# Optimization experiments

Measured on AMD Instinct MI355X. Metric: run time of the kernel, lower is better.

The kernel has to match this reference:

```python
import jax, jax.numpy as jnp
import numpy as np

D_MODEL = 2048
NUM_HEADS = 16
HEAD_DIM = D_MODEL // NUM_HEADS
BATCH = 2
SEQ = 2048


def setup_inputs() -> dict:
    key = jax.random.key(0)
    ks = jax.random.split(key, 5)
    s = 1.0 / np.sqrt(D_MODEL)
    return {
        "x": jax.random.normal(ks[0], (BATCH, SEQ, D_MODEL), dtype=jnp.float32),
        "Wq": jax.random.normal(ks[1], (D_MODEL, D_MODEL), dtype=jnp.float32) * s,
        "Wk": jax.random.normal(ks[2], (D_MODEL, D_MODEL), dtype=jnp.float32) * s,
        "Wv": jax.random.normal(ks[3], (D_MODEL, D_MODEL), dtype=jnp.float32) * s,
        "Wo": jax.random.normal(ks[4], (D_MODEL, D_MODEL), dtype=jnp.float32) * s,
    }


def reference(x, Wq, Wk, Wv, Wo):
    B, S, D = x.shape
    H, Dh = NUM_HEADS, HEAD_DIM
    # nn.Linear(bias=False): y = x @ W.T ; split_heads is a plain view (no transpose!)
    Q = (x @ Wq.T).reshape(B, H, S, Dh)
    K = (x @ Wk.T).reshape(B, H, S, Dh)
    V = (x @ Wv.T).reshape(B, H, S, Dh)
    # scores scaled by head_dim (NOT sqrt) — faithful to source
    scores = jnp.einsum("bhqd,bhkd->bhqk", Q, K) / jnp.float32(Dh)
    causal_mask = jnp.triu(jnp.ones((S, S), dtype=bool), k=1)  # True above diagonal
    scores = jnp.where(causal_mask, -jnp.inf, scores)
    attn = jax.nn.softmax(scores, axis=-1)
    out = jnp.einsum("bhqk,bhkd->bhqd", attn, V)  # [B,H,S,Dh]
    out = out.transpose(0, 2, 1, 3).reshape(B, S, D)  # merge DOES transpose
    return out @ Wo.T
```

## Files before the change

### kernel.cpp

```cpp
#include <hip/hip_runtime.h>
#include <hip/hip_bf16.h>

using bf16 = __hip_bfloat16;
typedef __attribute__((ext_vector_type(8))) short bf16x8;
typedef __attribute__((ext_vector_type(4))) float f32x4;

#define DEVI __device__ __forceinline__

constexpr int Bn = 2, Sn = 2048, Dn = 2048, Hn = 16, DHn = 128;
constexpr int Mn = Bn * Sn;

DEVI void gload_lds16(const bf16* g, bf16* l) {
  __builtin_amdgcn_global_load_lds(
      (__attribute__((address_space(1))) void*)g,
      (__attribute__((address_space(3))) void*)l,
      16, 0, 0);
}

__global__ __launch_bounds__(256) void cvt_bf16_k(const float* __restrict__ in,
                                                  bf16* __restrict__ out, int n8) {
  int i = blockIdx.x * 256 + threadIdx.x;
  if (i >= n8) return;
  const float4* p = (const float4*)in + (size_t)i * 2;
  float4 a = p[0], b = p[1];
  union { bf16 h[8]; bf16x8 v; } u;
  u.h[0] = __float2bfloat16(a.x); u.h[1] = __float2bfloat16(a.y);
  u.h[2] = __float2bfloat16(a.z); u.h[3] = __float2bfloat16(a.w);
  u.h[4] = __float2bfloat16(b.x); u.h[5] = __float2bfloat16(b.y);
  u.h[6] = __float2bfloat16(b.z); u.h[7] = __float2bfloat16(b.w);
  *((bf16x8*)out + i) = u.v;
}

template <int OUTF32, int NTOT, int NMAT>
__global__ __launch_bounds__(256, 2) void gemmY(const bf16* __restrict__ A,
                                                const bf16* __restrict__ W,
                                                void* __restrict__ Cv) {
  constexpr int K = 2048, BK = 32, NT = K / BK;
  __shared__ bf16 smem[2 * 12288];

  const int nwg = NTOT * 16;
  const int orig = blockIdx.x;
  const int wgid = (orig & 7) * (nwg >> 3) + (orig >> 3);
  const int bm = wgid / NTOT;
  const int bnn = wgid % NTOT;
  constexpr int nper = NTOT / NMAT;
  const int z = bnn / nper;
  const int col0 = (bnn % nper) * 128;

  const int t = threadIdx.x;
  const int wave = t >> 6, lane = t & 63;
  const int wm = wave >> 1, wn = wave & 1;
  const int lr = lane & 15, lg = lane >> 4;
  const int rch = ((lg ^ ((lr >> 1) & 3)) * 8);
  const int srow = t >> 2;
  const int sch = (t & 3) ^ ((t >> 3) & 3);

  const bf16* Ab = A + (size_t)(bm * 256 + srow) * K + sch * 8;
  const bf16* Bb = W + (size_t)z * (2048 * 2048) +
                   (size_t)(col0 + srow) * K + sch * 8;

  auto stgA = [&](int slot, int kt, int u) {
    gload_lds16(Ab + (size_t)u * 64 * K + kt * 32,
                smem + slot * 12288 + u * 2048 + t * 8);
  };
  auto stgB = [&](int slot, int kt, int v) {
    gload_lds16(Bb + (size_t)v * 64 * K + kt * 32,
                smem + slot * 12288 + 8192 + v * 2048 + t * 8);
  };

  f32x4 acc[8][4];
  const f32x4 zf = {0.f, 0.f, 0.f, 0.f};
#pragma unroll
  for (int i = 0; i < 8; ++i)
#pragma unroll
    for (int j = 0; j < 4; ++j) acc[i][j] = zf;

  stgA(0, 0, 0); stgA(0, 0, 1); stgA(0, 0, 2); stgA(0, 0, 3);
  stgB(0, 0, 0); stgB(0, 0, 1);
  stgA(1, 1, 0); stgA(1, 1, 2); stgB(1, 1, 0); stgB(1, 1, 1);

#pragma unroll 2
  for (int kt = 0; kt < NT; ++kt) {
    const int slot = kt & 1;
    const bf16* sAb = smem + slot * 12288;
    const bf16* sBb = sAb + 8192;

    if (kt == NT - 1) asm volatile("s_waitcnt vmcnt(0)" ::: "memory");
    else              asm volatile("s_waitcnt vmcnt(4)" ::: "memory");
    __builtin_amdgcn_s_barrier();

    bf16x8 af[4], bv[4];
#pragma unroll
    for (int i = 0; i < 4; ++i)
      af[i] = *(const bf16x8*)(sAb + (wm * 128 + i * 16 + lr) * 32 + rch);
#pragma unroll
    for (int n = 0; n < 4; ++n)
      bv[n] = *(const bf16x8*)(sBb + (wn * 64 + n * 16 + lr) * 32 + rch);
    if (kt + 1 < NT) { stgA(slot ^ 1, kt + 1, 1); stgA(slot ^ 1, kt + 1, 3); }
    asm volatile("s_waitcnt lgkmcnt(0)" ::: "memory");
    __builtin_amdgcn_sched_barrier(0);
    __builtin_amdgcn_s_setprio(1);
#pragma unroll
    for (int i = 0; i < 4; ++i)
#pragma unroll
      for (int n = 0; n < 4; ++n)
        acc[i][n] = __builtin_amdgcn_mfma_f32_16x16x32_bf16(af[i], bv[n], acc[i][n], 0, 0, 0);
    __builtin_amdgcn_s_setprio(0);
    __builtin_amdgcn_s_barrier();

#pragma unroll
    for (int i = 0; i < 4; ++i)
      af[i] = *(const bf16x8*)(sAb + (wm * 128 + 64 + i * 16 + lr) * 32 + rch);
    if (kt + 2 < NT) {
      stgA(slot, kt + 2, 0); stgA(slot, kt + 2, 2);
      stgB(slot, kt + 2, 0); stgB(slot, kt + 2, 1);
    }
    asm volatile("s_waitcnt lgkmcnt(0)" ::: "memory");
    __builtin_amdgcn_sched_barrier(0);
    __builtin_amdgcn_s_setprio(1);
#pragma unroll
    for (int i = 0; i < 4; ++i)
#pragma unroll
      for (int n = 0; n < 4; ++n)
        acc[4 + i][n] = __builtin_amdgcn_mfma_f32_16x16x32_bf16(af[i], bv[n], acc[4 + i][n], 0, 0, 0);
    __builtin_amdgcn_s_setprio(0);
  }

  const int r0 = bm * 256 + wm * 128, c0 = col0 + wn * 64;
#pragma unroll
  for (int mm = 0; mm < 8; ++mm)
#pragma unroll
    for (int nn = 0; nn < 4; ++nn) {
      const int rr = r0 + mm * 16 + lg * 4;
      const int cc = c0 + nn * 16 + lr;
#pragma unroll
      for (int r = 0; r < 4; ++r) {
        float v = acc[mm][nn][r];
        if (OUTF32) {
          ((float*)Cv)[(size_t)(rr + r) * 2048 + cc] = v;
        } else {
          bf16* C = (bf16*)Cv + (size_t)z * (Mn * 2048);
          C[(size_t)(rr + r) * 2048 + cc] = __float2bfloat16(v);
        }
      }
    }
}

__global__ __launch_bounds__(256, 2) void transpose_v(const bf16* __restrict__ V,
                                                      bf16* __restrict__ VT) {
  __shared__ bf16 tile[128 * 128];
  const int kt = blockIdx.x, bh = blockIdx.y;
  const bf16* Vh = V + (size_t)bh * (Sn * DHn);
  bf16* VTh = VT + (size_t)bh * (DHn * Sn);
  const int t = threadIdx.x;
  const int rr = t >> 4, cc = t & 15;
#pragma unroll
  for (int i = 0; i < 8; ++i) {
    int r = rr + i * 16;
    int ch = cc ^ ((r >> 3) & 7);
    *(bf16x8*)(tile + r * 128 + ch * 8) =
        *(const bf16x8*)(Vh + (size_t)(kt * 128 + r) * DHn + cc * 8);
  }
  __syncthreads();
  const int dr = t >> 4, li = t & 15;
#pragma unroll
  for (int i = 0; i < 8; ++i) {
    int dh = dr + i * 16;
    union { bf16 h[8]; bf16x8 v; } u;
#pragma unroll
    for (int j = 0; j < 8; ++j) {
      int k = li * 8 + j;
      int ch = (dh >> 3) ^ ((k >> 3) & 7);
      u.h[j] = tile[k * 128 + ch * 8 + (dh & 7)];
    }
    *(bf16x8*)(VTh + (size_t)dh * Sn + kt * 128 + li * 8) = u.v;
  }
}

__global__ __launch_bounds__(512, 1) void attn_k3(const bf16* __restrict__ Q,
                                                  const bf16* __restrict__ K,
                                                  const bf16* __restrict__ VT,
                                                  bf16* __restrict__ Mg) {
  __shared__ bf16 smem[40960];
  bf16* sK0 = smem;
  bf16* sK1 = smem + 8192;
  bf16* sV0 = smem + 16384;
  bf16* sV1 = smem + 24576;
  bf16* sP  = smem + 32768;
  bf16* sO  = smem;

  const int j = blockIdx.x;
  const int bh = blockIdx.y;
  const bf16* Qh = Q + (size_t)bh * (Sn * DHn);
  const bf16* Kh = K + (size_t)bh * (Sn * DHn);
  const bf16* VTh = VT + (size_t)bh * (DHn * Sn);
  const int b = bh >> 4, h = bh & 15;

  const int t = threadIdx.x, wave = t >> 6, lane = t & 63;
  const int lr = lane & 15, lg = lane >> 4;

  auto STAGE = [&](int buf, int kt) {
    bf16* dK = buf ? sK1 : sK0;
    bf16* dV = buf ? sV1 : sV0;
#pragma unroll
    for (int i = 0; i < 2; ++i) {
      int c = i * 512 + t;
      int row = c >> 4, c16 = c & 15;
      gload_lds16(Kh + (size_t)(kt * 64 + row) * DHn + ((c16 ^ (row & 7)) * 8),
                  dK + c * 8);
    }
#pragma unroll
    for (int i = 0; i < 2; ++i) {
      int c = i * 512 + t;
      int row = c >> 3, c8 = c & 7;
      gload_lds16(VTh + (size_t)row * Sn + kt * 64 + ((c8 ^ (row & 7)) * 8),
                  dV + c * 8);
    }
  };

  const f32x4 zf = {0.f, 0.f, 0.f, 0.f};

  for (int pi = 0; pi < 2; ++pi) {
    const int qb = pi ? (15 - j) : j;
    const int nt = qb * 2 + 2;
    const int q0 = qb * 128 + wave * 16;

    bf16x8 qf[4];
#pragma unroll
    for (int kk = 0; kk < 4; ++kk)
      qf[kk] = *(const bf16x8*)(Qh + (size_t)(q0 + lr) * DHn + kk * 32 + lg * 8);

    f32x4 o[8];
#pragma unroll
    for (int d = 0; d < 8; ++d) o[d] = zf;
    float mrun[4], lrun[4];
#pragma unroll
    for (int r = 0; r < 4; ++r) { mrun[r] = -3e38f; lrun[r] = 0.f; }

    STAGE(0, 0);
    __syncthreads();
    int cur = 0;

    for (int kt = 0; kt < nt; ++kt) {
      if (kt + 1 < nt) STAGE(cur ^ 1, kt + 1);

      bf16* sKc = cur ? sK1 : sK0;
      bf16* sVc = cur ? sV1 : sV0;

      f32x4 sfr[4];
#pragma unroll
      for (int nn = 0; nn < 4; ++nn) sfr[nn] = zf;
#pragma unroll
      for (int kk = 0; kk < 4; ++kk)
#pragma unroll
        for (int nn = 0; nn < 4; ++nn) {
          int row = nn * 16 + lr;
          int ch = (kk * 4 + lg) ^ (row & 7);
          bf16x8 kf = *(const bf16x8*)(sKc + row * DHn + ch * 8);
          sfr[nn] = __builtin_amdgcn_mfma_f32_16x16x32_bf16(qf[kk], kf, sfr[nn], 0, 0, 0);
        }

      const bool maskt = (kt >= qb * 2);
      float pv[4][4];
#pragma unroll
      for (int nn = 0; nn < 4; ++nn)
#pragma unroll
        for (int r = 0; r < 4; ++r) {
          float v = sfr[nn][r] * (1.0f / 128.0f);
          if (maskt) {
            int kg = kt * 64 + nn * 16 + lr;
            int qg = q0 + lg * 4 + r;
            if (kg > qg) v = -1e30f;
          }
          pv[nn][r] = v;
        }
      float mnew[4], alpha[4], rsum[4];
#pragma unroll
      for (int r = 0; r < 4; ++r) {
        float rm = fmaxf(fmaxf(pv[0][r], pv[1][r]), fmaxf(pv[2][r], pv[3][r]));
        rm = fmaxf(rm, __shfl_xor(rm, 1));
        rm = fmaxf(rm, __shfl_xor(rm, 2));
        rm = fmaxf(rm, __shfl_xor(rm, 4));
        rm = fmaxf(rm, __shfl_xor(rm, 8));
        mnew[r] = fmaxf(mrun[r], rm);
        alpha[r] = __expf(mrun[r] - mnew[r]);
        mrun[r] = mnew[r];
        rsum[r] = 0.f;
      }
#pragma unroll
      for (int nn = 0; nn < 4; ++nn)
#pragma unroll
        for (int r = 0; r < 4; ++r) {
          float p = __expf(pv[nn][r] - mnew[r]);
          pv[nn][r] = p;
          rsum[r] += p;
        }
#pragma unroll
      for (int r = 0; r < 4; ++r) {
        float s = rsum[r];
        s += __shfl_xor(s, 1); s += __shfl_xor(s, 2);
        s += __shfl_xor(s, 4); s += __shfl_xor(s, 8);
        lrun[r] = lrun[r] * alpha[r] + s;
      }
#pragma unroll
      for (int d = 0; d < 8; ++d)
#pragma unroll
        for (int r = 0; r < 4; ++r) o[d][r] *= alpha[r];

#pragma unroll
      for (int nn = 0; nn < 4; ++nn)
#pragma unroll
        for (int r = 0; r < 4; ++r) {
          int row = lg * 4 + r;
          int chk = (nn * 2 + (lr >> 3)) ^ (row & 7);
          sP[wave * 1024 + row * 64 + chk * 8 + (lr & 7)] = __float2bfloat16(pv[nn][r]);
        }

      bf16x8 pf[2];
#pragma unroll
      for (int kk = 0; kk < 2; ++kk) {
        int ch = (kk * 4 + lg) ^ (lr & 7);
        pf[kk] = *(const bf16x8*)(sP + wave * 1024 + lr * 64 + ch * 8);
      }
#pragma unroll
      for (int d = 0; d < 8; ++d)
#pragma unroll
        for (int kk = 0; kk < 2; ++kk) {
          int vrow = d * 16 + lr;
          int vch = (kk * 4 + lg) ^ (vrow & 7);
          bf16x8 vf = *(const bf16x8*)(sVc + vrow * 64 + vch * 8);
          o[d] = __builtin_amdgcn_mfma_f32_16x16x32_bf16(pf[kk], vf, o[d], 0, 0, 0);
        }

      __syncthreads();
      cur ^= 1;
    }

    float inv[4];
#pragma unroll
    for (int r = 0; r < 4; ++r) inv[r] = 1.0f / lrun[r];
#pragma unroll
    for (int d = 0; d < 8; ++d)
#pragma unroll
      for (int r = 0; r < 4; ++r) {
        int row = wave * 16 + lg * 4 + r;
        int col = d * 16 + lr;
        int chk = ((col >> 3) ^ (row & 7));
        sO[row * 128 + chk * 8 + (col & 7)] = __float2bfloat16(o[d][r] * inv[r]);
      }
    __syncthreads();
    bf16* Mh = Mg + ((size_t)(b * Sn + qb * 128)) * Dn + h * DHn;
#pragma unroll
    for (int i = 0; i < 4; ++i) {
      int row = (t >> 4) + i * 32;
      int c16 = t & 15;
      *(bf16x8*)(Mh + (size_t)row * Dn + c16 * 8) =
          *(const bf16x8*)(sO + row * 128 + ((c16 ^ (row & 7)) * 8));
    }
    __syncthreads();
  }
}

extern "C" void kernel_launch(void* const* d_in, const int* in_sizes, int n_in,
                              void* d_out, int out_size, void* d_ws, size_t ws_size,
                              hipStream_t stream) {
  const float* x = (const float*)d_in[0];
  const float* Wq = (const float*)d_in[1];
  const float* Wk = (const float*)d_in[2];
  const float* Wv = (const float*)d_in[3];
  const float* Wo = (const float*)d_in[4];
  float* out = (float*)d_out;

  char* ws = (char*)d_ws;
  bf16* xb = (bf16*)ws;            ws += (size_t)Mn * Dn * 2;
  bf16* Wb = (bf16*)ws;            ws += (size_t)4 * Dn * Dn * 2;
  bf16* QKV = (bf16*)ws;           ws += (size_t)3 * Mn * Dn * 2;
  bf16* VT = (bf16*)ws;            ws += (size_t)Bn * Hn * DHn * Sn * 2;
  bf16* Mg = (bf16*)ws;            ws += (size_t)Mn * Dn * 2;

  const int nx8 = Mn * Dn / 8;
  const int nw8 = Dn * Dn / 8;
  cvt_bf16_k<<<nx8 / 256, 256, 0, stream>>>(x, xb, nx8);
  cvt_bf16_k<<<nw8 / 256, 256, 0, stream>>>(Wq, Wb + 0 * (size_t)Dn * Dn, nw8);
  cvt_bf16_k<<<nw8 / 256, 256, 0, stream>>>(Wk, Wb + 1 * (size_t)Dn * Dn, nw8);
  cvt_bf16_k<<<nw8 / 256, 256, 0, stream>>>(Wv, Wb + 2 * (size_t)Dn * Dn, nw8);
  cvt_bf16_k<<<nw8 / 256, 256, 0, stream>>>(Wo, Wb + 3 * (size_t)Dn * Dn, nw8);

  gemmY<0, 48, 3><<<768, 256, 0, stream>>>(xb, Wb, (void*)QKV);

  transpose_v<<<dim3(16, 32), 256, 0, stream>>>(QKV + 2 * (size_t)Mn * Dn, VT);

  attn_k3<<<dim3(8, 32), 512, 0, stream>>>(QKV, QKV + (size_t)Mn * Dn, VT, Mg);

  gemmY<1, 16, 1><<<256, 256, 0, stream>>>(Mg, Wb + 3 * (size_t)Dn * Dn, (void*)out);
}
```

Measured before the change: 262.5 us.

## Parameterize GEMM M-tile and simplify pipeline; use 128-row tiles for output projection

Generalizes the GEMM kernel over the M tile height (MW), switches to a simple double-buffered loop that prefetches the whole next K-slice at once and waits with vmcnt(0), and drops the split half-tile MFMA phases. The QKV projection keeps 256-row tiles while the output projection moves to 128-row tiles, doubling its grid to 512 workgroups to fill the CUs better. The simpler pipeline gives up the finer-grained overlap of loads and MFMAs in exchange for fewer barriers.

```diff
diff --git a/kernel.cpp b/kernel.cpp
--- a/kernel.cpp
+++ b/kernel.cpp
@@ -31,14 +31,17 @@
   *((bf16x8*)out + i) = u.v;
 }
 
-template <int OUTF32, int NTOT, int NMAT>
-__global__ __launch_bounds__(256, 2) void gemmY(const bf16* __restrict__ A,
+template <int OUTF32, int NTOT, int NMAT, int MW>
+__global__ __launch_bounds__(256, 2) void gemmZ(const bf16* __restrict__ A,
                                                 const bf16* __restrict__ W,
                                                 void* __restrict__ Cv) {
-  constexpr int K = 2048, BK = 32, NT = K / BK;
-  __shared__ bf16 smem[2 * 12288];
-
-  const int nwg = NTOT * 16;
+  constexpr int K = 2048, NT = K / 32;
+  constexpr int BM = MW * 32;
+  constexpr int SLOT = (BM + 128) * 32;
+  __shared__ bf16 smem[2 * SLOT];
+
+  constexpr int MT = Mn / BM;
+  const int nwg = NTOT * MT;
   const int orig = blockIdx.x;
   const int wgid = (orig & 7) * (nwg >> 3) + (orig >> 3);
   const int bm = wgid / NTOT;
@@ -55,80 +58,68 @@
   const int srow = t >> 2;
   const int sch = (t & 3) ^ ((t >> 3) & 3);
 
-  const bf16* Ab = A + (size_t)(bm * 256 + srow) * K + sch * 8;
+  const bf16* Ab = A + (size_t)(bm * BM + srow) * K + sch * 8;
   const bf16* Bb = W + (size_t)z * (2048 * 2048) +
                    (size_t)(col0 + srow) * K + sch * 8;
 
   auto stgA = [&](int slot, int kt, int u) {
     gload_lds16(Ab + (size_t)u * 64 * K + kt * 32,
-                smem + slot * 12288 + u * 2048 + t * 8);
+                smem + slot * SLOT + u * 2048 + t * 8);
   };
   auto stgB = [&](int slot, int kt, int v) {
     gload_lds16(Bb + (size_t)v * 64 * K + kt * 32,
-                smem + slot * 12288 + 8192 + v * 2048 + t * 8);
+                smem + slot * SLOT + BM * 32 + v * 2048 + t * 8);
   };
 
-  f32x4 acc[8][4];
+  f32x4 acc[MW][4];
   const f32x4 zf = {0.f, 0.f, 0.f, 0.f};
 #pragma unroll
-  for (int i = 0; i < 8; ++i)
+  for (int i = 0; i < MW; ++i)
 #pragma unroll
     for (int j = 0; j < 4; ++j) acc[i][j] = zf;
 
-  stgA(0, 0, 0); stgA(0, 0, 1); stgA(0, 0, 2); stgA(0, 0, 3);
+#pragma unroll
+  for (int u = 0; u < MW / 2; ++u) stgA(0, 0, u);
   stgB(0, 0, 0); stgB(0, 0, 1);
-  stgA(1, 1, 0); stgA(1, 1, 2); stgB(1, 1, 0); stgB(1, 1, 1);
 
 #pragma unroll 2
   for (int kt = 0; kt < NT; ++kt) {
     const int slot = kt & 1;
-    const bf16* sAb = smem + slot * 12288;
-    const bf16* sBb = sAb + 8192;
-
-    if (kt == NT - 1) asm volatile("s_waitcnt vmcnt(0)" ::: "memory");
-    else              asm volatile("s_waitcnt vmcnt(4)" ::: "memory");
+    const bf16* sAb = smem + slot * SLOT;
+    const bf16* sBb = sAb + BM * 32;
+
+    asm volatile("s_waitcnt vmcnt(0)" ::: "memory");
+    __builtin_amdgcn_sched_barrier(0);
     __builtin_amdgcn_s_barrier();
-
-    bf16x8 af[4], bv[4];
-#pragma unroll
-    for (int i = 0; i < 4; ++i)
-      af[i] = *(const bf16x8*)(sAb + (wm * 128 + i * 16 + lr) * 32 + rch);
+    __builtin_amdgcn_sched_barrier(0);
+
+    if (kt + 1 < NT) {
+#pragma unroll
+      for (int u = 0; u < MW / 2; ++u) stgA(slot ^ 1, kt + 1, u);
+      stgB(slot ^ 1, kt + 1, 0); stgB(slot ^ 1, kt + 1, 1);
+    }
+
+    bf16x8 bv[4], af[MW];
 #pragma unroll
     for (int n = 0; n < 4; ++n)
       bv[n] = *(const bf16x8*)(sBb + (wn * 64 + n * 16 + lr) * 32 + rch);
-    if (kt + 1 < NT) { stgA(slot ^ 1, kt + 1, 1); stgA(slot ^ 1, kt + 1, 3); }
-    asm volatile("s_waitcnt lgkmcnt(0)" ::: "memory");
-    __builtin_amdgcn_sched_barrier(0);
+#pragma unroll
+    for (int i = 0; i < MW; ++i)
+      af[i] = *(const bf16x8*)(sAb + (wm * (MW * 16) + i * 16 + lr) * 32 + rch);
+
     __builtin_amdgcn_s_setprio(1);
 #pragma unroll
-    for (int i = 0; i < 4; ++i)
+    for (int i = 0; i < MW; ++i)
 #pragma unroll
       for (int n = 0; n < 4; ++n)
         acc[i][n] = __builtin_amdgcn_mfma_f32_16x16x32_bf16(af[i], bv[n], acc[i][n], 0, 0, 0);
     __builtin_amdgcn_s_setprio(0);
-    __builtin_amdgcn_s_barrier();
-
-#pragma unroll
-    for (int i = 0; i < 4; ++i)
-      af[i] = *(const bf16x8*)(sAb + (wm * 128 + 64 + i * 16 + lr) * 32 + rch);
-    if (kt + 2 < NT) {
-      stgA(slot, kt + 2, 0); stgA(slot, kt + 2, 2);
-      stgB(slot, kt + 2, 0); stgB(slot, kt + 2, 1);
-    }
-    asm volatile("s_waitcnt lgkmcnt(0)" ::: "memory");
     __builtin_amdgcn_sched_barrier(0);
-    __builtin_amdgcn_s_setprio(1);
-#pragma unroll
-    for (int i = 0; i < 4; ++i)
-#pragma unroll
-      for (int n = 0; n < 4; ++n)
-        acc[4 + i][n] = __builtin_amdgcn_mfma_f32_16x16x32_bf16(af[i], bv[n], acc[4 + i][n], 0, 0, 0);
-    __builtin_amdgcn_s_setprio(0);
   }
 
-  const int r0 = bm * 256 + wm * 128, c0 = col0 + wn * 64;
-#pragma unroll
-  for (int mm = 0; mm < 8; ++mm)
+  const int r0 = bm * BM + wm * (MW * 16), c0 = col0 + wn * 64;
+#pragma unroll
+  for (int mm = 0; mm < MW; ++mm)
 #pragma unroll
     for (int nn = 0; nn < 4; ++nn) {
       const int rr = r0 + mm * 16 + lg * 4;
@@ -386,11 +377,11 @@
   cvt_bf16_k<<<nw8 / 256, 256, 0, stream>>>(Wv, Wb + 2 * (size_t)Dn * Dn, nw8);
   cvt_bf16_k<<<nw8 / 256, 256, 0, stream>>>(Wo, Wb + 3 * (size_t)Dn * Dn, nw8);
 
-  gemmY<0, 48, 3><<<768, 256, 0, stream>>>(xb, Wb, (void*)QKV);
+  gemmZ<0, 48, 3, 8><<<768, 256, 0, stream>>>(xb, Wb, (void*)QKV);
 
   transpose_v<<<dim3(16, 32), 256, 0, stream>>>(QKV + 2 * (size_t)Mn * Dn, VT);
 
   attn_k3<<<dim3(8, 32), 512, 0, stream>>>(QKV, QKV + (size_t)Mn * Dn, VT, Mg);
 
-  gemmY<1, 16, 1><<<256, 256, 0, stream>>>(Mg, Wb + 3 * (size_t)Dn * Dn, (void*)out);
-}
+  gemmZ<1, 16, 1, 4><<<512, 256, 0, stream>>>(Mg, Wb + 3 * (size_t)Dn * Dn, (void*)out);
+}
```

Result: slower. 268.7 us (+2.4%).

## Split-K output projection, fuse conversion launches, remap attention blocks across XCDs

Applied to the files above, without the earlier changes.

The five fp32-to-bf16 conversion launches are merged into one grid-strided kernel. The output projection GEMM is split along K into two halves, each writing fp32 partials into the reused QKV buffer, followed by a reduction kernel. This doubles the block count from 256 and should fill the GPU better. The attention grid is flattened and remapped so that blocks for the same head land on the same XCD for L2 locality. The cost is extra fp32 partial traffic plus one more launch for the reduction.

```diff
diff --git a/kernel.cpp b/kernel.cpp
--- a/kernel.cpp
+++ b/kernel.cpp
@@ -17,25 +17,40 @@
       16, 0, 0);
 }
 
-__global__ __launch_bounds__(256) void cvt_bf16_k(const float* __restrict__ in,
-                                                  bf16* __restrict__ out, int n8) {
-  int i = blockIdx.x * 256 + threadIdx.x;
-  if (i >= n8) return;
-  const float4* p = (const float4*)in + (size_t)i * 2;
-  float4 a = p[0], b = p[1];
-  union { bf16 h[8]; bf16x8 v; } u;
-  u.h[0] = __float2bfloat16(a.x); u.h[1] = __float2bfloat16(a.y);
-  u.h[2] = __float2bfloat16(a.z); u.h[3] = __float2bfloat16(a.w);
-  u.h[4] = __float2bfloat16(b.x); u.h[5] = __float2bfloat16(b.y);
-  u.h[6] = __float2bfloat16(b.z); u.h[7] = __float2bfloat16(b.w);
-  *((bf16x8*)out + i) = u.v;
-}
-
-template <int OUTF32, int NTOT, int NMAT>
+__global__ __launch_bounds__(256) void cvt_all_k(const float* __restrict__ x,
+                                                 const float* __restrict__ wq,
+                                                 const float* __restrict__ wk,
+                                                 const float* __restrict__ wv,
+                                                 const float* __restrict__ wo,
+                                                 bf16* __restrict__ xb,
+                                                 bf16* __restrict__ wb) {
+  const int which = blockIdx.y;
+  const float* src;
+  bf16* dst;
+  int n8;
+  if (which == 0) { src = x;  dst = xb; n8 = Mn * Dn / 8; }
+  else {
+    src = (which == 1) ? wq : (which == 2) ? wk : (which == 3) ? wv : wo;
+    dst = wb + (size_t)(which - 1) * Dn * Dn;
+    n8 = Dn * Dn / 8;
+  }
+  for (int i = blockIdx.x * 256 + threadIdx.x; i < n8; i += gridDim.x * 256) {
+    const float4* p = (const float4*)src + (size_t)i * 2;
+    float4 a = p[0], b = p[1];
+    union { bf16 h[8]; bf16x8 v; } u;
+    u.h[0] = __float2bfloat16(a.x); u.h[1] = __float2bfloat16(a.y);
+    u.h[2] = __float2bfloat16(a.z); u.h[3] = __float2bfloat16(a.w);
+    u.h[4] = __float2bfloat16(b.x); u.h[5] = __float2bfloat16(b.y);
+    u.h[6] = __float2bfloat16(b.z); u.h[7] = __float2bfloat16(b.w);
+    *((bf16x8*)dst + i) = u.v;
+  }
+}
+
+template <int MODE, int NTOT, int NMAT, int NTK>
 __global__ __launch_bounds__(256, 2) void gemmY(const bf16* __restrict__ A,
                                                 const bf16* __restrict__ W,
                                                 void* __restrict__ Cv) {
-  constexpr int K = 2048, BK = 32, NT = K / BK;
+  constexpr int K = 2048;
   __shared__ bf16 smem[2 * 12288];
 
   const int nwg = NTOT * 16;
@@ -46,6 +61,7 @@
   constexpr int nper = NTOT / NMAT;
   const int z = bnn / nper;
   const int col0 = (bnn % nper) * 128;
+  const int kbase = (MODE == 1) ? (int)blockIdx.z * (NTK * 32) : 0;
 
   const int t = threadIdx.x;
   const int wave = t >> 6, lane = t & 63;
@@ -55,9 +71,9 @@
   const int srow = t >> 2;
   const int sch = (t & 3) ^ ((t >> 3) & 3);
 
-  const bf16* Ab = A + (size_t)(bm * 256 + srow) * K + sch * 8;
+  const bf16* Ab = A + (size_t)(bm * 256 + srow) * K + kbase + sch * 8;
   const bf16* Bb = W + (size_t)z * (2048 * 2048) +
-                   (size_t)(col0 + srow) * K + sch * 8;
+                   (size_t)(col0 + srow) * K + kbase + sch * 8;
 
   auto stgA = [&](int slot, int kt, int u) {
     gload_lds16(Ab + (size_t)u * 64 * K + kt * 32,
@@ -80,13 +96,13 @@
   stgA(1, 1, 0); stgA(1, 1, 2); stgB(1, 1, 0); stgB(1, 1, 1);
 
 #pragma unroll 2
-  for (int kt = 0; kt < NT; ++kt) {
+  for (int kt = 0; kt < NTK; ++kt) {
     const int slot = kt & 1;
     const bf16* sAb = smem + slot * 12288;
     const bf16* sBb = sAb + 8192;
 
-    if (kt == NT - 1) asm volatile("s_waitcnt vmcnt(0)" ::: "memory");
-    else              asm volatile("s_waitcnt vmcnt(4)" ::: "memory");
+    if (kt == NTK - 1) asm volatile("s_waitcnt vmcnt(0)" ::: "memory");
+    else               asm volatile("s_waitcnt vmcnt(4)" ::: "memory");
     __builtin_amdgcn_s_barrier();
 
     bf16x8 af[4], bv[4];
@@ -96,7 +112,7 @@
 #pragma unroll
     for (int n = 0; n < 4; ++n)
       bv[n] = *(const bf16x8*)(sBb + (wn * 64 + n * 16 + lr) * 32 + rch);
-    if (kt + 1 < NT) { stgA(slot ^ 1, kt + 1, 1); stgA(slot ^ 1, kt + 1, 3); }
+    if (kt + 1 < NTK) { stgA(slot ^ 1, kt + 1, 1); stgA(slot ^ 1, kt + 1, 3); }
     asm volatile("s_waitcnt lgkmcnt(0)" ::: "memory");
     __builtin_amdgcn_sched_barrier(0);
     __builtin_amdgcn_s_setprio(1);
@@ -111,7 +127,7 @@
 #pragma unroll
     for (int i = 0; i < 4; ++i)
       af[i] = *(const bf16x8*)(sAb + (wm * 128 + 64 + i * 16 + lr) * 32 + rch);
-    if (kt + 2 < NT) {
+    if (kt + 2 < NTK) {
       stgA(slot, kt + 2, 0); stgA(slot, kt + 2, 2);
       stgB(slot, kt + 2, 0); stgB(slot, kt + 2, 1);
     }
@@ -136,14 +152,26 @@
 #pragma unroll
       for (int r = 0; r < 4; ++r) {
         float v = acc[mm][nn][r];
-        if (OUTF32) {
-          ((float*)Cv)[(size_t)(rr + r) * 2048 + cc] = v;
+        if (MODE == 1) {
+          float* P = (float*)Cv + (size_t)blockIdx.z * (Mn * 2048);
+          P[(size_t)(rr + r) * 2048 + cc] = v;
         } else {
           bf16* C = (bf16*)Cv + (size_t)z * (Mn * 2048);
           C[(size_t)(rr + r) * 2048 + cc] = __float2bfloat16(v);
         }
       }
     }
+}
+
+__global__ __launch_bounds__(256) void reduce_k(const float* __restrict__ P,
+                                                float* __restrict__ out, int n4) {
+  const float4* P0 = (const float4*)P;
+  const float4* P1 = (const float4*)(P + (size_t)Mn * 2048);
+  float4* O = (float4*)out;
+  for (int i = blockIdx.x * 256 + threadIdx.x; i < n4; i += gridDim.x * 256) {
+    float4 a = P0[i], b = P1[i];
+    O[i] = make_float4(a.x + b.x, a.y + b.y, a.z + b.z, a.w + b.w);
+  }
 }
 
 __global__ __launch_bounds__(256, 2) void transpose_v(const bf16* __restrict__ V,
@@ -189,8 +217,10 @@
   bf16* sP  = smem + 32768;
   bf16* sO  = smem;
 
-  const int j = blockIdx.x;
-  const int bh = blockIdx.y;
+  const int bi = blockIdx.x;
+  const int xcd = bi & 7, slt = bi >> 3;
+  const int bh = (slt & 3) * 8 + xcd;
+  const int j = slt >> 2;
   const bf16* Qh = Q + (size_t)bh * (Sn * DHn);
   const bf16* Kh = K + (size_t)bh * (Sn * DHn);
   const bf16* VTh = VT + (size_t)bh * (DHn * Sn);
@@ -377,20 +407,16 @@
   bf16* QKV = (bf16*)ws;           ws += (size_t)3 * Mn * Dn * 2;
   bf16* VT = (bf16*)ws;            ws += (size_t)Bn * Hn * DHn * Sn * 2;
   bf16* Mg = (bf16*)ws;            ws += (size_t)Mn * Dn * 2;
-
-  const int nx8 = Mn * Dn / 8;
-  const int nw8 = Dn * Dn / 8;
-  cvt_bf16_k<<<nx8 / 256, 256, 0, stream>>>(x, xb, nx8);
-  cvt_bf16_k<<<nw8 / 256, 256, 0, stream>>>(Wq, Wb + 0 * (size_t)Dn * Dn, nw8);
-  cvt_bf16_k<<<nw8 / 256, 256, 0, stream>>>(Wk, Wb + 1 * (size_t)Dn * Dn, nw8);
-  cvt_bf16_k<<<nw8 / 256, 256, 0, stream>>>(Wv, Wb + 2 * (size_t)Dn * Dn, nw8);
-  cvt_bf16_k<<<nw8 / 256, 256, 0, stream>>>(Wo, Wb + 3 * (size_t)Dn * Dn, nw8);
-
-  gemmY<0, 48, 3><<<768, 256, 0, stream>>>(xb, Wb, (void*)QKV);
+  float* Pk = (float*)QKV;
+
+  cvt_all_k<<<dim3(2048, 5), 256, 0, stream>>>(x, Wq, Wk, Wv, Wo, xb, Wb);
+
+  gemmY<0, 48, 3, 64><<<768, 256, 0, stream>>>(xb, Wb, (void*)QKV);
 
   transpose_v<<<dim3(16, 32), 256, 0, stream>>>(QKV + 2 * (size_t)Mn * Dn, VT);
 
-  attn_k3<<<dim3(8, 32), 512, 0, stream>>>(QKV, QKV + (size_t)Mn * Dn, VT, Mg);
-
-  gemmY<1, 16, 1><<<256, 256, 0, stream>>>(Mg, Wb + 3 * (size_t)Dn * Dn, (void*)out);
-}
+  attn_k3<<<256, 512, 0, stream>>>(QKV, QKV + (size_t)Mn * Dn, VT, Mg);
+
+  gemmY<1, 16, 1, 32><<<dim3(256, 1, 2), 256, 0, stream>>>(Mg, Wb + 3 * (size_t)Dn * Dn, (void*)Pk);
+  reduce_k<<<2048, 256, 0, stream>>>(Pk, out, Mn * Dn / 4);
+}
```

Result: no change. 266.6 us (+1.6%).
